# Kernel optimization log

Measured on AMD Instinct MI355X. Metric: run time of the kernel, lower is better.

Reference implementation:

```python
import jax, jax.numpy as jnp
import numpy as np

DIM = 128
NUM_HEADS = 4
HEAD_DIM = DIM // NUM_HEADS
WS = 8            # window height/width
SHIFT = 4
N_CAND = 4        # candidates per spatial position
H_RES, W_RES = 64, 128
M = WS * WS       # tokens per window spatially
L = M * N_CAND    # window sequence length
NW = (H_RES // WS) * (W_RES // WS)
B = 1
B_ = NW * B
NEG_INF = -1e9  # finite stand-in for -inf; softmax result identical within fp tolerance


def _rel_position_index():
    ch = np.arange(WS); cw = np.arange(WS)
    coords = np.stack(np.meshgrid(ch, cw, indexing='ij')).reshape(2, -1)  # [2, M]
    rel = (coords[:, :, None] - coords[:, None, :]).transpose(1, 2, 0)    # [M, M, 2]
    rel = rel + np.array([WS - 1, WS - 1])
    rel[..., 0] *= 2 * WS - 1
    return rel.sum(-1).astype(np.int32)  # [M, M] in [0, (2WS-1)^2)


def _window_attn_mask():
    # block message passing between same spatial position's candidates (except self)
    idx = np.repeat(np.arange(M), N_CAND).astype(np.float64)  # [L]
    m = idx[:, None] - idx[None, :]
    mask = np.where(m == 0, NEG_INF, 0.0)
    mask[np.arange(L), np.arange(L)] = 0.0
    return mask  # [L, L]


def _shift_window_attn_mask():
    img = np.zeros((H_RES, W_RES))
    cnt = 0
    for hs in (slice(0, -WS), slice(-WS, -SHIFT), slice(-SHIFT, None)):
        for ws in (slice(0, -WS), slice(-WS, -SHIFT), slice(-SHIFT, None)):
            img[hs, ws] = cnt
            cnt += 1
    mw = img.reshape(H_RES // WS, WS, W_RES // WS, WS).transpose(0, 2, 1, 3).reshape(-1, M)  # [nW, M]
    am = mw[:, None, :] - mw[:, :, None]           # [nW, M, M]
    am = np.where(am != 0, NEG_INF, 0.0)
    am = np.repeat(np.repeat(am, N_CAND, axis=1), N_CAND, axis=2)  # [nW, L, L]
    return am + _window_attn_mask()[None]


def setup_inputs() -> dict:
    key = jax.random.key(0)
    ks = jax.random.split(key, 6)
    x = jax.random.normal(ks[0], (B_, L, DIM), dtype=jnp.float32)
    qkv_w = jax.random.normal(ks[1], (3 * DIM, DIM), dtype=jnp.float32) * 0.02
    qkv_b = jnp.zeros((3 * DIM,), dtype=jnp.float32)
    rpe_table = jax.random.normal(ks[2], ((2 * WS - 1) ** 2, 3 * DIM), dtype=jnp.float32) * 0.02
    proj_w = jax.random.normal(ks[3], (DIM, DIM), dtype=jnp.float32) * 0.02
    proj_b = jnp.zeros((DIM,), dtype=jnp.float32)
    attn_mask = jnp.asarray(_shift_window_attn_mask(), dtype=jnp.float32)
    rel_idx = jnp.asarray(_rel_position_index())
    return {"x": x, "qkv_w": qkv_w, "qkv_b": qkv_b, "rpe_table": rpe_table,
            "proj_w": proj_w, "proj_b": proj_b, "attn_mask": attn_mask, "rel_idx": rel_idx}


def reference(x, qkv_w, qkv_b, rpe_table, proj_w, proj_b, attn_mask, rel_idx):
    b_, l, _ = x.shape
    h, hd = NUM_HEADS, HEAD_DIM
    scale = hd ** -0.5
    # QKV projection -> [B_, h, L, hd] each
    qkv = (x @ qkv_w.T + qkv_b).reshape(b_, l, 3, h, hd).transpose(2, 0, 3, 1, 4)
    q, k, v = qkv[0], qkv[1], qkv[2]
    # relative-position encodings gathered per (i, j) pair, expanded over candidates
    m = rel_idx.shape[0]
    n = l // m
    rpe = rpe_table[rel_idx.reshape(-1)].reshape(m, m, h, 3 * hd)
    rpe = jnp.repeat(jnp.repeat(rpe, n, axis=0), n, axis=1)  # [L, L, h, 3*hd]
    q_rpe, k_rpe, v_rpe = jnp.split(rpe, 3, axis=-1)
    q = q * scale
    q_rpe = q_rpe * scale
    qk = jnp.einsum('bhic,bhjc->bhij', q, k)
    qr = jnp.einsum('bhic,ijhc->bhij', q, k_rpe)
    kr = jnp.einsum('bhjc,ijhc->bhij', k, q_rpe)
    attn = qk + qr + kr  # [B_, h, L, L]
    nw = attn_mask.shape[0]
    attn = attn.reshape(b_ // nw, nw, h, l, l) + attn_mask[None, :, None]
    attn = attn.reshape(b_, h, l, l)
    attn = jax.nn.softmax(attn.astype(jnp.float32), axis=-1).astype(x.dtype)
    out = jnp.einsum('bhij,bhjc->bhic', attn, v) + jnp.einsum('bhij,ijhc->bhic', attn, v_rpe)
    out = out.transpose(0, 2, 1, 3).reshape(b_, l, DIM)
    return out @ proj_w.T + proj_b
```

## Files before the change

kernel.cpp:

```cpp
#include <hip/hip_runtime.h>
#include <math.h>

constexpr int HD    = 32;
constexpr int LW    = 256;
constexpr int NWIN  = 128;
constexpr int ROWS  = NWIN * LW;
constexpr int QKVC  = 384;
constexpr float SCALE = 0.17677669529663687f;

typedef __attribute__((ext_vector_type(8))) short short8;
typedef __attribute__((ext_vector_type(4))) float f32x4;
union I4S8 { int4 i; short8 s; };

__device__ inline float dot4(const float4 a, const float4 b) {
  return a.x * b.x + a.y * b.y + a.z * b.z + a.w * b.w;
}

__device__ inline unsigned short f2bf(float f) {
  unsigned u = __float_as_uint(f);
  unsigned r = (u + 0x7FFFu + ((u >> 16) & 1u)) >> 16;
  return (unsigned short)r;
}

__global__ __launch_bounds__(256) void cast_x4_kernel(
    const float* __restrict__ in, unsigned short* __restrict__ out, int n4)
{
  int i = blockIdx.x * 256 + threadIdx.x;
  if (i >= n4) return;
  float4 v = ((const float4*)in)[i];
  ushort4 o;
  o.x = f2bf(v.x); o.y = f2bf(v.y); o.z = f2bf(v.z); o.w = f2bf(v.w);
  ((ushort4*)out)[i] = o;
}

__global__ __launch_bounds__(256) void rpe_gather_kernel(
    const float* __restrict__ tab, const int* __restrict__ rel_idx,
    float* __restrict__ out)
{
  int gid = blockIdx.x * 256 + threadIdx.x;
  int s   = gid % 96;
  int hp  = gid / 96;
  int p   = hp & 4095;
  int h   = hp >> 12;
  float v = tab[(size_t)rel_idx[p] * 384 + h * 96 + s];
  if (s < 32) v *= SCALE;
  out[gid] = v;
}

template <int N>
__global__ __launch_bounds__(256) void gemm_mfma_bt(
    const unsigned short* __restrict__ A, const unsigned short* __restrict__ W,
    const float* __restrict__ bias, float* __restrict__ C)
{
  constexpr int K   = 128;
  constexpr int LDI = 28;
  __shared__ int As[128 * LDI];
  __shared__ int Bs[128 * LDI];
  const int tid  = threadIdx.x;
  const int wave = tid >> 6;
  const int lane = tid & 63;
  const int lm   = lane & 15;
  const int q    = lane >> 4;
  const int m0   = blockIdx.x * 128;
  const int n0   = blockIdx.y * 128;

  const int* Ag = (const int*)(A + (size_t)m0 * K);
  const int* Wg = (const int*)(W + (size_t)n0 * K);

  const int srow = tid >> 2;
  const int sk4  = (tid & 3) * 4;

  f32x4 acc[2][8] = {};

  for (int ks = 0; ks < 4; ++ks) {
    const int goff = ks * 16 + sk4;
    int4 a0 = *(const int4*)(Ag + (size_t)srow * 64 + goff);
    int4 a1 = *(const int4*)(Ag + (size_t)(srow + 64) * 64 + goff);
    int4 w0 = *(const int4*)(Wg + (size_t)srow * 64 + goff);
    int4 w1 = *(const int4*)(Wg + (size_t)(srow + 64) * 64 + goff);
    *(int4*)&As[srow * LDI + sk4]        = a0;
    *(int4*)&As[(srow + 64) * LDI + sk4] = a1;
    *(int4*)&Bs[srow * LDI + sk4]        = w0;
    *(int4*)&Bs[(srow + 64) * LDI + sk4] = w1;
    __syncthreads();

    short8 af[2], bf[8];
#pragma unroll
    for (int t = 0; t < 2; ++t) {
      const int m = (wave * 2 + t) * 16 + lm;
      I4S8 u; u.i = *(const int4*)&As[m * LDI + q * 4];
      af[t] = u.s;
    }
#pragma unroll
    for (int nt = 0; nt < 8; ++nt) {
      const int n = nt * 16 + lm;
      I4S8 u; u.i = *(const int4*)&Bs[n * LDI + q * 4];
      bf[nt] = u.s;
    }
#pragma unroll
    for (int t = 0; t < 2; ++t)
#pragma unroll
      for (int nt = 0; nt < 8; ++nt)
        acc[t][nt] = __builtin_amdgcn_mfma_f32_16x16x32_bf16(
            af[t], bf[nt], acc[t][nt], 0, 0, 0);
    __syncthreads();
  }

#pragma unroll
  for (int t = 0; t < 2; ++t) {
    const int mrow = m0 + (wave * 2 + t) * 16 + q * 4;
#pragma unroll
    for (int nt = 0; nt < 8; ++nt) {
      const int col = n0 + nt * 16 + lm;
      const float bb = bias[col];
#pragma unroll
      for (int r = 0; r < 4; ++r)
        C[(size_t)(mrow + r) * N + col] = acc[t][nt][r] + bb;
    }
  }
}

__global__ __launch_bounds__(512) void attn_kernel(
    const float* __restrict__ qkv, const float* __restrict__ rpeg,
    const float* __restrict__ mask, unsigned short* __restrict__ out)
{
  __shared__ float ms[256 * 33];
  const int b = blockIdx.x;
  const int h = blockIdx.y;
  const int tid = threadIdx.x;
  const int row = tid & 255;
  const int jh  = __builtin_amdgcn_readfirstlane(tid >> 8);
  const size_t rowbase = (size_t)b * LW;

  const float* kvbase = qkv + rowbase * QKVC + 128 + h * HD;

  float4 q[8];
  {
    const float4* qr = (const float4*)(qkv + (rowbase + row) * QKVC + h * HD);
#pragma unroll
    for (int d = 0; d < 8; ++d) {
      float4 t = qr[d];
      q[d] = make_float4(t.x * SCALE, t.y * SCALE, t.z * SCALE, t.w * SCALE);
    }
  }
  const float4* rp4base =
      (const float4*)(rpeg + ((size_t)h * 4096 + (size_t)(row >> 2) * 64) * 96);
  const float* mrow = mask + ((size_t)b * LW + row) * LW;

  float4 acc[8];
#pragma unroll
  for (int d = 0; d < 8; ++d) acc[d] = make_float4(0.f, 0.f, 0.f, 0.f);
  float l_run = 0.f;
  const int jbase = jh << 5;

  for (int l = 0; l < 32; ++l) {
    const int j4 = jbase + l;
    const float4* rp = rp4base + j4 * 24;
    float4 uq[8];
    float c0 = 0.f;
#pragma unroll
    for (int d = 0; d < 8; ++d) {
      float4 sq = rp[d];
      float4 kr = rp[8 + d];
      uq[d] = make_float4(q[d].x + sq.x, q[d].y + sq.y,
                          q[d].z + sq.z, q[d].w + sq.w);
      c0 += dot4(q[d], kr);
    }
    float4 mv = *(const float4*)(mrow + j4 * 4);
    const float* kj0 = kvbase + (size_t)(j4 * 4) * QKVC;
    float s[4] = {mv.x + c0, mv.y + c0, mv.z + c0, mv.w + c0};
#pragma unroll
    for (int jc = 0; jc < 4; ++jc) {
      const float4* kj = (const float4*)(kj0 + jc * QKVC);
      float sa = 0.f;
#pragma unroll
      for (int d = 0; d < 8; ++d) sa += dot4(uq[d], kj[d]);
      s[jc] += sa;
    }
    float p[4];
    p[0] = __expf(s[0]); p[1] = __expf(s[1]);
    p[2] = __expf(s[2]); p[3] = __expf(s[3]);
    float pool = (p[0] + p[1]) + (p[2] + p[3]);
    l_run += pool;
#pragma unroll
    for (int jc = 0; jc < 4; ++jc) {
      const float4* vj = (const float4*)(kj0 + jc * QKVC + 128);
      float pj = p[jc];
#pragma unroll
      for (int d = 0; d < 8; ++d) {
        acc[d].x += pj * vj[d].x; acc[d].y += pj * vj[d].y;
        acc[d].z += pj * vj[d].z; acc[d].w += pj * vj[d].w;
      }
    }
#pragma unroll
    for (int d = 0; d < 8; ++d) {
      float4 vr = rp[16 + d];
      acc[d].x += pool * vr.x; acc[d].y += pool * vr.y;
      acc[d].z += pool * vr.z; acc[d].w += pool * vr.w;
    }
  }

  __syncthreads();
  if (jh == 1) {
    float* dst = &ms[row * 33];
#pragma unroll
    for (int d = 0; d < 8; ++d) {
      dst[d * 4 + 0] = acc[d].x; dst[d * 4 + 1] = acc[d].y;
      dst[d * 4 + 2] = acc[d].z; dst[d * 4 + 3] = acc[d].w;
    }
    dst[32] = l_run;
  }
  __syncthreads();
  if (jh == 0) {
    const float* src = &ms[row * 33];
    float inv = 1.f / (l_run + src[32]);
    unsigned short* orow = out + (rowbase + row) * 128 + h * HD;
#pragma unroll
    for (int d = 0; d < 8; ++d) {
      ushort4 r;
      r.x = f2bf((acc[d].x + src[d * 4 + 0]) * inv);
      r.y = f2bf((acc[d].y + src[d * 4 + 1]) * inv);
      r.z = f2bf((acc[d].z + src[d * 4 + 2]) * inv);
      r.w = f2bf((acc[d].w + src[d * 4 + 3]) * inv);
      *(ushort4*)(orow + d * 4) = r;
    }
  }
}

extern "C" void kernel_launch(void* const* d_in, const int* in_sizes, int n_in,
                              void* d_out, int out_size, void* d_ws, size_t ws_size,
                              hipStream_t stream) {
  (void)in_sizes; (void)n_in; (void)out_size; (void)ws_size;
  const float* x         = (const float*)d_in[0];
  const float* qkv_w     = (const float*)d_in[1];
  const float* qkv_b     = (const float*)d_in[2];
  const float* rpe_table = (const float*)d_in[3];
  const float* proj_w    = (const float*)d_in[4];
  const float* proj_b    = (const float*)d_in[5];
  const float* attn_mask = (const float*)d_in[6];
  const int*   rel_idx   = (const int*)d_in[7];
  float* out = (float*)d_out;

  float* qkvbuf = (float*)d_ws;
  float* rpeg   = qkvbuf + (size_t)ROWS * QKVC;
  unsigned short* xbf    = (unsigned short*)(rpeg + (size_t)4 * 4096 * 96);
  unsigned short* qkvwbf = xbf + (size_t)ROWS * 128;
  unsigned short* projwbf= qkvwbf + (size_t)QKVC * 128;
  unsigned short* attnbf = projwbf + (size_t)128 * 128;

  hipLaunchKernelGGL(cast_x4_kernel, dim3(ROWS * 128 / 4 / 256), dim3(256), 0,
                     stream, x, xbf, ROWS * 128 / 4);
  hipLaunchKernelGGL(cast_x4_kernel, dim3(48), dim3(256), 0, stream,
                     qkv_w, qkvwbf, QKVC * 128 / 4);
  hipLaunchKernelGGL(cast_x4_kernel, dim3(16), dim3(256), 0, stream,
                     proj_w, projwbf, 128 * 128 / 4);
  hipLaunchKernelGGL(rpe_gather_kernel, dim3(6144), dim3(256), 0, stream,
                     rpe_table, rel_idx, rpeg);

  hipLaunchKernelGGL((gemm_mfma_bt<QKVC>), dim3(ROWS / 128, QKVC / 128),
                     dim3(256), 0, stream, xbf, qkvwbf, qkv_b, qkvbuf);
  hipLaunchKernelGGL(attn_kernel, dim3(NWIN, 4), dim3(512), 0, stream,
                     qkvbuf, rpeg, attn_mask, attnbf);
  hipLaunchKernelGGL((gemm_mfma_bt<128>), dim3(ROWS / 128, 1),
                     dim3(256), 0, stream, attnbf, projwbf, proj_b, out);
}
```

Before: 325.9 us.

## Decompose RPE attention into precomputed bias terms and MFMA score/PV kernel

Replaces the scalar fp32 attention kernel with a pipeline of separate kernels. The QKV GEMM now writes scaled Q, K and a transposed V in bf16, split per head. Two new kernels precompute the q·k_rpe and k·q_rpe bias tables. An MFMA kernel then computes QK^T and P·V, derives the shift-window and candidate mask from window indices instead of reading the mask tensor, and writes pooled probabilities. A finish kernel adds the v_rpe contribution and normalizes. The goal is to move the dominant FLOPs onto matrix cores and drop the 32MB mask read, at the cost of several large intermediate buffers and extra bf16 rounding of scores and biases.

```diff
diff --git a/kernel.cpp b/kernel.cpp
--- a/kernel.cpp
+++ b/kernel.cpp
@@ -1,7 +1,6 @@
 #include <hip/hip_runtime.h>
 #include <math.h>
 
-constexpr int HD    = 32;
 constexpr int LW    = 256;
 constexpr int NWIN  = 128;
 constexpr int ROWS  = NWIN * LW;
@@ -12,14 +11,12 @@
 typedef __attribute__((ext_vector_type(4))) float f32x4;
 union I4S8 { int4 i; short8 s; };
 
-__device__ inline float dot4(const float4 a, const float4 b) {
-  return a.x * b.x + a.y * b.y + a.z * b.z + a.w * b.w;
-}
-
 __device__ inline unsigned short f2bf(float f) {
   unsigned u = __float_as_uint(f);
-  unsigned r = (u + 0x7FFFu + ((u >> 16) & 1u)) >> 16;
-  return (unsigned short)r;
+  return (unsigned short)((u + 0x7FFFu + ((u >> 16) & 1u)) >> 16);
+}
+__device__ inline float bf2f(unsigned short s) {
+  return __uint_as_float(((unsigned)s) << 16);
 }
 
 __global__ __launch_bounds__(256) void cast_x4_kernel(
@@ -47,31 +44,25 @@
   out[gid] = v;
 }
 
-template <int N>
-__global__ __launch_bounds__(256) void gemm_mfma_bt(
+__global__ __launch_bounds__(256) void qkv_gemm(
     const unsigned short* __restrict__ A, const unsigned short* __restrict__ W,
-    const float* __restrict__ bias, float* __restrict__ C)
-{
-  constexpr int K   = 128;
-  constexpr int LDI = 28;
+    const float* __restrict__ bias,
+    unsigned short* __restrict__ qsbf, unsigned short* __restrict__ Kbf,
+    unsigned short* __restrict__ Vtg)
+{
+  constexpr int K = 128, LDI = 28;
   __shared__ int As[128 * LDI];
   __shared__ int Bs[128 * LDI];
-  const int tid  = threadIdx.x;
-  const int wave = tid >> 6;
-  const int lane = tid & 63;
-  const int lm   = lane & 15;
-  const int q    = lane >> 4;
-  const int m0   = blockIdx.x * 128;
-  const int n0   = blockIdx.y * 128;
-
+  const int tid = threadIdx.x, wave = tid >> 6, lane = tid & 63;
+  const int lm = lane & 15, q = lane >> 4;
+  const int m0 = blockIdx.x * 128;
+  const int region = blockIdx.y;
+  const int n0 = region * 128;
   const int* Ag = (const int*)(A + (size_t)m0 * K);
   const int* Wg = (const int*)(W + (size_t)n0 * K);
-
-  const int srow = tid >> 2;
-  const int sk4  = (tid & 3) * 4;
+  const int srow = tid >> 2, sk4 = (tid & 3) * 4;
 
   f32x4 acc[2][8] = {};
-
   for (int ks = 0; ks < 4; ++ks) {
     const int goff = ks * 16 + sk4;
     int4 a0 = *(const int4*)(Ag + (size_t)srow * 64 + goff);
@@ -83,7 +74,6 @@
     *(int4*)&Bs[srow * LDI + sk4]        = w0;
     *(int4*)&Bs[(srow + 64) * LDI + sk4] = w1;
     __syncthreads();
-
     short8 af[2], bf[8];
 #pragma unroll
     for (int t = 0; t < 2; ++t) {
@@ -105,7 +95,257 @@
             af[t], bf[nt], acc[t][nt], 0, 0, 0);
     __syncthreads();
   }
-
+#pragma unroll
+  for (int t = 0; t < 2; ++t) {
+#pragma unroll
+    for (int nt = 0; nt < 8; ++nt) {
+      const int c = nt * 16 + lm, hh = c >> 5, d = c & 31;
+      const float bb = bias[n0 + c];
+#pragma unroll
+      for (int r = 0; r < 4; ++r) {
+        const int ig = m0 + (wave * 2 + t) * 16 + q * 4 + r;
+        const int b = ig >> 8, i = ig & 255;
+        const size_t bh = (size_t)(b * 4 + hh);
+        const float v = acc[t][nt][r] + bb;
+        if (region == 0)      qsbf[(bh * 256 + i) * 32 + d] = f2bf(v * SCALE);
+        else if (region == 1) Kbf[(bh * 256 + i) * 32 + d]  = f2bf(v);
+        else                  Vtg[(bh * 32 + d) * 256 + i]  = f2bf(v);
+      }
+    }
+  }
+}
+
+__global__ __launch_bounds__(256) void c0_kernel(
+    const unsigned short* __restrict__ qsbf, const float* __restrict__ rpeg,
+    unsigned short* __restrict__ c0g)
+{
+  const int blk = blockIdx.x;
+  const int bq = blk & 7, hj = blk >> 3, h = hj >> 6, j4 = hj & 63;
+  const int b = bq * 16 + (threadIdx.x >> 4);
+  const int i0 = (threadIdx.x & 15) * 16;
+  const size_t bh = (size_t)(b * 4 + h);
+  unsigned short outb[16];
+  for (int ii = 0; ii < 16; ++ii) {
+    const int i = i0 + ii;
+    const float* kr = rpeg + ((size_t)h * 4096 + (size_t)(i >> 2) * 64 + j4) * 96 + 32;
+    const unsigned short* qr = qsbf + (bh * 256 + i) * 32;
+    float s = 0.f;
+#pragma unroll
+    for (int d4 = 0; d4 < 8; ++d4) {
+      ushort4 u = *(const ushort4*)(qr + d4 * 4);
+      float4 k = *(const float4*)(kr + d4 * 4);
+      s += bf2f(u.x) * k.x + bf2f(u.y) * k.y + bf2f(u.z) * k.z + bf2f(u.w) * k.w;
+    }
+    outb[ii] = f2bf(s);
+  }
+  unsigned short* dst = c0g + (((size_t)h * 128 + b) * 64 + j4) * 256 + i0;
+  *(int4*)(dst)     = *(int4*)&outb[0];
+  *(int4*)(dst + 8) = *(int4*)&outb[8];
+}
+
+__global__ __launch_bounds__(256) void t2_kernel(
+    const unsigned short* __restrict__ Kbf, const float* __restrict__ rpeg,
+    unsigned short* __restrict__ t2g)
+{
+  const int blk = blockIdx.x;
+  const int bq = blk & 7, hi = blk >> 3, h = hi >> 6, i4 = hi & 63;
+  const int b = bq * 16 + (threadIdx.x >> 4);
+  const int jg = threadIdx.x & 15;
+  const size_t bh = (size_t)(b * 4 + h);
+  unsigned short outb[16];
+  for (int jj = 0; jj < 16; ++jj) {
+    const int j = jg * 16 + jj;
+    const float* sq = rpeg + ((size_t)h * 4096 + (size_t)i4 * 64 + (j >> 2)) * 96;
+    const unsigned short* krow = Kbf + (bh * 256 + j) * 32;
+    float s = 0.f;
+#pragma unroll
+    for (int d4 = 0; d4 < 8; ++d4) {
+      ushort4 u = *(const ushort4*)(krow + d4 * 4);
+      float4 k = *(const float4*)(sq + d4 * 4);
+      s += bf2f(u.x) * k.x + bf2f(u.y) * k.y + bf2f(u.z) * k.z + bf2f(u.w) * k.w;
+    }
+    outb[jj] = f2bf(s);
+  }
+  unsigned short* dst = t2g + (((size_t)h * 128 + b) * 64 + i4) * 256 + jg * 16;
+  *(int4*)(dst)     = *(int4*)&outb[0];
+  *(int4*)(dst + 8) = *(int4*)&outb[8];
+}
+
+__global__ __launch_bounds__(1024) void attn_mfma(
+    const unsigned short* __restrict__ qsbf, const unsigned short* __restrict__ Kbf,
+    const unsigned short* __restrict__ Vtg, const unsigned short* __restrict__ c0g,
+    const unsigned short* __restrict__ t2g,
+    float* __restrict__ O_raw, float* __restrict__ lbuf,
+    unsigned short* __restrict__ poolg)
+{
+  __shared__ float Plds[16 * 576];
+  const int b = blockIdx.x, h = blockIdx.y;
+  const int tid = threadIdx.x, wave = tid >> 6, lane = tid & 63;
+  const int q = lane >> 4, lm = lane & 15;
+  const size_t bh = (size_t)(b * 4 + h);
+  const int ibase = wave * 16;
+
+  short8 qfrag;
+  { I4S8 u; u.i = *(const int4*)(qsbf + (bh * 256 + ibase + lm) * 32 + q * 8);
+    qfrag = u.s; }
+
+  const int bh7 = ((b >> 4) == 7) ? 1 : 0;
+  const int bw15 = ((b & 15) == 15) ? 1 : 0;
+  int ii[4], rid_i[4];
+#pragma unroll
+  for (int r = 0; r < 4; ++r) {
+    const int i = ibase + q * 4 + r; ii[r] = i;
+    const int m = i >> 2, mh = m >> 3, mw = m & 7;
+    rid_i[r] = (bh7 ? (mh >= 4 ? 2 : 1) : 0) * 3 + (bw15 ? (mw >= 4 ? 2 : 1) : 0);
+  }
+
+  f32x4 acc0 = {0.f, 0.f, 0.f, 0.f}, acc1 = {0.f, 0.f, 0.f, 0.f};
+  float lp[4] = {0.f, 0.f, 0.f, 0.f};
+  float* Pw = Plds + wave * 576;
+  const unsigned short* Kb  = Kbf + bh * 8192;
+  const unsigned short* Vb  = Vtg + bh * 8192;
+  const unsigned short* c0b = c0g + (size_t)(h * 128 + b) * 16384;
+  const unsigned short* t2b = t2g + (size_t)(h * 128 + b) * 16384;
+
+  for (int it = 0; it < 8; ++it) {
+    const int jb = it * 32;
+#pragma unroll
+    for (int jtt = 0; jtt < 2; ++jtt) {
+      const int jcol = jb + jtt * 16;
+      const int j = jcol + lm;
+      I4S8 ku; ku.i = *(const int4*)(Kb + j * 32 + q * 8);
+      f32x4 z = {0.f, 0.f, 0.f, 0.f};
+      f32x4 sacc = __builtin_amdgcn_mfma_f32_16x16x32_bf16(qfrag, ku.s, z, 0, 0, 0);
+      const int mj = j >> 2, mjh = mj >> 3, mjw = mj & 7;
+      const int rid_j =
+          (bh7 ? (mjh >= 4 ? 2 : 1) : 0) * 3 + (bw15 ? (mjw >= 4 ? 2 : 1) : 0);
+#pragma unroll
+      for (int r = 0; r < 4; ++r) {
+        const int i = ii[r];
+        float s = sacc[r] + bf2f(c0b[mj * 256 + i]) + bf2f(t2b[(i >> 2) * 256 + j]);
+        const bool blocked = (rid_i[r] != rid_j) || (((i >> 2) == mj) && (i != j));
+        float p = blocked ? 0.f : __expf(s);
+        lp[r] += p;
+        float pl = p + __shfl_xor(p, 1);
+        pl += __shfl_xor(pl, 2);
+        if ((lm & 3) == 0)
+          poolg[(bh * 256 + i) * 64 + (jcol >> 2) + (lm >> 2)] = f2bf(pl);
+        Pw[(q * 4 + r) * 36 + jtt * 16 + lm] = p;
+      }
+    }
+    float4 pfa = *(const float4*)(Pw + lm * 36 + q * 8);
+    float4 pfb = *(const float4*)(Pw + lm * 36 + q * 8 + 4);
+    short8 pa;
+    pa[0] = (short)f2bf(pfa.x); pa[1] = (short)f2bf(pfa.y);
+    pa[2] = (short)f2bf(pfa.z); pa[3] = (short)f2bf(pfa.w);
+    pa[4] = (short)f2bf(pfb.x); pa[5] = (short)f2bf(pfb.y);
+    pa[6] = (short)f2bf(pfb.z); pa[7] = (short)f2bf(pfb.w);
+    { I4S8 v0; v0.i = *(const int4*)(Vb + lm * 256 + jb + q * 8);
+      acc0 = __builtin_amdgcn_mfma_f32_16x16x32_bf16(pa, v0.s, acc0, 0, 0, 0);
+      I4S8 v1; v1.i = *(const int4*)(Vb + (16 + lm) * 256 + jb + q * 8);
+      acc1 = __builtin_amdgcn_mfma_f32_16x16x32_bf16(pa, v1.s, acc1, 0, 0, 0); }
+  }
+
+#pragma unroll
+  for (int r = 0; r < 4; ++r) {
+    float l = lp[r];
+    l += __shfl_xor(l, 1); l += __shfl_xor(l, 2);
+    l += __shfl_xor(l, 4); l += __shfl_xor(l, 8);
+    if (lm == 0) lbuf[bh * 256 + ii[r]] = l;
+    O_raw[(bh * 256 + ii[r]) * 32 + lm]      = acc0[r];
+    O_raw[(bh * 256 + ii[r]) * 32 + 16 + lm] = acc1[r];
+  }
+}
+
+__global__ __launch_bounds__(256) void finish_kernel(
+    const float* __restrict__ O_raw, const float* __restrict__ lbuf,
+    const unsigned short* __restrict__ poolg, const float* __restrict__ rpeg,
+    unsigned short* __restrict__ attnbf)
+{
+  const int b = blockIdx.x, h = blockIdx.y, i = threadIdx.x;
+  const size_t bh = (size_t)(b * 4 + h);
+  const float inv = 1.f / lbuf[bh * 256 + i];
+  float pool[64];
+  { const ushort4* pp = (const ushort4*)(poolg + (bh * 256 + i) * 64);
+#pragma unroll
+    for (int t = 0; t < 16; ++t) {
+      ushort4 u = pp[t];
+      pool[t * 4 + 0] = bf2f(u.x); pool[t * 4 + 1] = bf2f(u.y);
+      pool[t * 4 + 2] = bf2f(u.z); pool[t * 4 + 3] = bf2f(u.w);
+    } }
+  float4 acc[8] = {};
+  const float* vbase = rpeg + ((size_t)h * 4096 + (size_t)(i >> 2) * 64) * 96 + 64;
+  for (int j4 = 0; j4 < 64; ++j4) {
+    const float pl = pool[j4];
+    const float4* vr = (const float4*)(vbase + (size_t)j4 * 96);
+#pragma unroll
+    for (int d4 = 0; d4 < 8; ++d4) {
+      float4 v = vr[d4];
+      acc[d4].x += pl * v.x; acc[d4].y += pl * v.y;
+      acc[d4].z += pl * v.z; acc[d4].w += pl * v.w;
+    }
+  }
+  const float4* orow = (const float4*)(O_raw + (bh * 256 + i) * 32);
+  unsigned short* dst = attnbf + ((size_t)b * 256 + i) * 128 + h * 32;
+#pragma unroll
+  for (int d4 = 0; d4 < 8; ++d4) {
+    float4 o = orow[d4];
+    ushort4 u;
+    u.x = f2bf((o.x + acc[d4].x) * inv);
+    u.y = f2bf((o.y + acc[d4].y) * inv);
+    u.z = f2bf((o.z + acc[d4].z) * inv);
+    u.w = f2bf((o.w + acc[d4].w) * inv);
+    *(ushort4*)(dst + d4 * 4) = u;
+  }
+}
+
+template <int N>
+__global__ __launch_bounds__(256) void gemm_mfma_bt(
+    const unsigned short* __restrict__ A, const unsigned short* __restrict__ W,
+    const float* __restrict__ bias, float* __restrict__ C)
+{
+  constexpr int K = 128, LDI = 28;
+  __shared__ int As[128 * LDI];
+  __shared__ int Bs[128 * LDI];
+  const int tid = threadIdx.x, wave = tid >> 6, lane = tid & 63;
+  const int lm = lane & 15, q = lane >> 4;
+  const int m0 = blockIdx.x * 128, n0 = blockIdx.y * 128;
+  const int* Ag = (const int*)(A + (size_t)m0 * K);
+  const int* Wg = (const int*)(W + (size_t)n0 * K);
+  const int srow = tid >> 2, sk4 = (tid & 3) * 4;
+  f32x4 acc[2][8] = {};
+  for (int ks = 0; ks < 4; ++ks) {
+    const int goff = ks * 16 + sk4;
+    int4 a0 = *(const int4*)(Ag + (size_t)srow * 64 + goff);
+    int4 a1 = *(const int4*)(Ag + (size_t)(srow + 64) * 64 + goff);
+    int4 w0 = *(const int4*)(Wg + (size_t)srow * 64 + goff);
+    int4 w1 = *(const int4*)(Wg + (size_t)(srow + 64) * 64 + goff);
+    *(int4*)&As[srow * LDI + sk4]        = a0;
+    *(int4*)&As[(srow + 64) * LDI + sk4] = a1;
+    *(int4*)&Bs[srow * LDI + sk4]        = w0;
+    *(int4*)&Bs[(srow + 64) * LDI + sk4] = w1;
+    __syncthreads();
+    short8 af[2], bf[8];
+#pragma unroll
+    for (int t = 0; t < 2; ++t) {
+      const int m = (wave * 2 + t) * 16 + lm;
+      I4S8 u; u.i = *(const int4*)&As[m * LDI + q * 4];
+      af[t] = u.s;
+    }
+#pragma unroll
+    for (int nt = 0; nt < 8; ++nt) {
+      const int n = nt * 16 + lm;
+      I4S8 u; u.i = *(const int4*)&Bs[n * LDI + q * 4];
+      bf[nt] = u.s;
+    }
+#pragma unroll
+    for (int t = 0; t < 2; ++t)
+#pragma unroll
+      for (int nt = 0; nt < 8; ++nt)
+        acc[t][nt] = __builtin_amdgcn_mfma_f32_16x16x32_bf16(
+            af[t], bf[nt], acc[t][nt], 0, 0, 0);
+    __syncthreads();
+  }
 #pragma unroll
   for (int t = 0; t < 2; ++t) {
     const int mrow = m0 + (wave * 2 + t) * 16 + q * 4;
@@ -116,113 +356,6 @@
 #pragma unroll
       for (int r = 0; r < 4; ++r)
         C[(size_t)(mrow + r) * N + col] = acc[t][nt][r] + bb;
-    }
-  }
-}
-
-__global__ __launch_bounds__(512) void attn_kernel(
-    const float* __restrict__ qkv, const float* __restrict__ rpeg,
-    const float* __restrict__ mask, unsigned short* __restrict__ out)
-{
-  __shared__ float ms[256 * 33];
-  const int b = blockIdx.x;
-  const int h = blockIdx.y;
-  const int tid = threadIdx.x;
-  const int row = tid & 255;
-  const int jh  = __builtin_amdgcn_readfirstlane(tid >> 8);
-  const size_t rowbase = (size_t)b * LW;
-
-  const float* kvbase = qkv + rowbase * QKVC + 128 + h * HD;
-
-  float4 q[8];
-  {
-    const float4* qr = (const float4*)(qkv + (rowbase + row) * QKVC + h * HD);
-#pragma unroll
-    for (int d = 0; d < 8; ++d) {
-      float4 t = qr[d];
-      q[d] = make_float4(t.x * SCALE, t.y * SCALE, t.z * SCALE, t.w * SCALE);
-    }
-  }
-  const float4* rp4base =
-      (const float4*)(rpeg + ((size_t)h * 4096 + (size_t)(row >> 2) * 64) * 96);
-  const float* mrow = mask + ((size_t)b * LW + row) * LW;
-
-  float4 acc[8];
-#pragma unroll
-  for (int d = 0; d < 8; ++d) acc[d] = make_float4(0.f, 0.f, 0.f, 0.f);
-  float l_run = 0.f;
-  const int jbase = jh << 5;
-
-  for (int l = 0; l < 32; ++l) {
-    const int j4 = jbase + l;
-    const float4* rp = rp4base + j4 * 24;
-    float4 uq[8];
-    float c0 = 0.f;
-#pragma unroll
-    for (int d = 0; d < 8; ++d) {
-      float4 sq = rp[d];
-      float4 kr = rp[8 + d];
-      uq[d] = make_float4(q[d].x + sq.x, q[d].y + sq.y,
-                          q[d].z + sq.z, q[d].w + sq.w);
-      c0 += dot4(q[d], kr);
-    }
-    float4 mv = *(const float4*)(mrow + j4 * 4);
-    const float* kj0 = kvbase + (size_t)(j4 * 4) * QKVC;
-    float s[4] = {mv.x + c0, mv.y + c0, mv.z + c0, mv.w + c0};
-#pragma unroll
-    for (int jc = 0; jc < 4; ++jc) {
-      const float4* kj = (const float4*)(kj0 + jc * QKVC);
-      float sa = 0.f;
-#pragma unroll
-      for (int d = 0; d < 8; ++d) sa += dot4(uq[d], kj[d]);
-      s[jc] += sa;
-    }
-    float p[4];
-    p[0] = __expf(s[0]); p[1] = __expf(s[1]);
-    p[2] = __expf(s[2]); p[3] = __expf(s[3]);
-    float pool = (p[0] + p[1]) + (p[2] + p[3]);
-    l_run += pool;
-#pragma unroll
-    for (int jc = 0; jc < 4; ++jc) {
-      const float4* vj = (const float4*)(kj0 + jc * QKVC + 128);
-      float pj = p[jc];
-#pragma unroll
-      for (int d = 0; d < 8; ++d) {
-        acc[d].x += pj * vj[d].x; acc[d].y += pj * vj[d].y;
-        acc[d].z += pj * vj[d].z; acc[d].w += pj * vj[d].w;
-      }
-    }
-#pragma unroll
-    for (int d = 0; d < 8; ++d) {
-      float4 vr = rp[16 + d];
-      acc[d].x += pool * vr.x; acc[d].y += pool * vr.y;
-      acc[d].z += pool * vr.z; acc[d].w += pool * vr.w;
-    }
-  }
-
-  __syncthreads();
-  if (jh == 1) {
-    float* dst = &ms[row * 33];
-#pragma unroll
-    for (int d = 0; d < 8; ++d) {
-      dst[d * 4 + 0] = acc[d].x; dst[d * 4 + 1] = acc[d].y;
-      dst[d * 4 + 2] = acc[d].z; dst[d * 4 + 3] = acc[d].w;
-    }
-    dst[32] = l_run;
-  }
-  __syncthreads();
-  if (jh == 0) {
-    const float* src = &ms[row * 33];
-    float inv = 1.f / (l_run + src[32]);
-    unsigned short* orow = out + (rowbase + row) * 128 + h * HD;
-#pragma unroll
-    for (int d = 0; d < 8; ++d) {
-      ushort4 r;
-      r.x = f2bf((acc[d].x + src[d * 4 + 0]) * inv);
-      r.y = f2bf((acc[d].y + src[d * 4 + 1]) * inv);
-      r.z = f2bf((acc[d].z + src[d * 4 + 2]) * inv);
-      r.w = f2bf((acc[d].w + src[d * 4 + 3]) * inv);
-      *(ushort4*)(orow + d * 4) = r;
     }
   }
 }
@@ -237,30 +370,42 @@
   const float* rpe_table = (const float*)d_in[3];
   const float* proj_w    = (const float*)d_in[4];
   const float* proj_b    = (const float*)d_in[5];
-  const float* attn_mask = (const float*)d_in[6];
   const int*   rel_idx   = (const int*)d_in[7];
   float* out = (float*)d_out;
 
-  float* qkvbuf = (float*)d_ws;
-  float* rpeg   = qkvbuf + (size_t)ROWS * QKVC;
-  unsigned short* xbf    = (unsigned short*)(rpeg + (size_t)4 * 4096 * 96);
-  unsigned short* qkvwbf = xbf + (size_t)ROWS * 128;
-  unsigned short* projwbf= qkvwbf + (size_t)QKVC * 128;
-  unsigned short* attnbf = projwbf + (size_t)128 * 128;
-
-  hipLaunchKernelGGL(cast_x4_kernel, dim3(ROWS * 128 / 4 / 256), dim3(256), 0,
-                     stream, x, xbf, ROWS * 128 / 4);
+  char* w = (char*)d_ws;
+  unsigned short* xbf     = (unsigned short*)w;            w += 8388608;
+  unsigned short* qkvwbf  = (unsigned short*)w;            w += 98304;
+  unsigned short* projwbf = (unsigned short*)w;            w += 32768;
+  float*          rpeg    = (float*)w;                     w += 6291456;
+  unsigned short* qsbf    = (unsigned short*)w;            w += 8388608;
+  unsigned short* Kbf     = (unsigned short*)w;            w += 8388608;
+  unsigned short* Vtg     = (unsigned short*)w;            w += 8388608;
+  unsigned short* c0g     = (unsigned short*)w;            w += 16777216;
+  unsigned short* t2g     = (unsigned short*)w;            w += 16777216;
+  unsigned short* poolg   = (unsigned short*)w;            w += 16777216;
+  float*          O_raw   = (float*)w;                     w += 16777216;
+  float*          lbuf    = (float*)w;                     w += 524288;
+  unsigned short* attnbf  = xbf;
+
+  hipLaunchKernelGGL(cast_x4_kernel, dim3(4096), dim3(256), 0, stream,
+                     x, xbf, ROWS * 128 / 4);
   hipLaunchKernelGGL(cast_x4_kernel, dim3(48), dim3(256), 0, stream,
                      qkv_w, qkvwbf, QKVC * 128 / 4);
   hipLaunchKernelGGL(cast_x4_kernel, dim3(16), dim3(256), 0, stream,
                      proj_w, projwbf, 128 * 128 / 4);
   hipLaunchKernelGGL(rpe_gather_kernel, dim3(6144), dim3(256), 0, stream,
                      rpe_table, rel_idx, rpeg);
-
-  hipLaunchKernelGGL((gemm_mfma_bt<QKVC>), dim3(ROWS / 128, QKVC / 128),
-                     dim3(256), 0, stream, xbf, qkvwbf, qkv_b, qkvbuf);
-  hipLaunchKernelGGL(attn_kernel, dim3(NWIN, 4), dim3(512), 0, stream,
-                     qkvbuf, rpeg, attn_mask, attnbf);
-  hipLaunchKernelGGL((gemm_mfma_bt<128>), dim3(ROWS / 128, 1),
-                     dim3(256), 0, stream, attnbf, projwbf, proj_b, out);
-}
+  hipLaunchKernelGGL(qkv_gemm, dim3(ROWS / 128, 3), dim3(256), 0, stream,
+                     xbf, qkvwbf, qkv_b, qsbf, Kbf, Vtg);
+  hipLaunchKernelGGL(c0_kernel, dim3(2048), dim3(256), 0, stream,
+                     qsbf, rpeg, c0g);
+  hipLaunchKernelGGL(t2_kernel, dim3(2048), dim3(256), 0, stream,
+                     Kbf, rpeg, t2g);
+  hipLaunchKernelGGL(attn_mfma, dim3(NWIN, 4), dim3(1024), 0, stream,
+                     qsbf, Kbf, Vtg, c0g, t2g, O_raw, lbuf, poolg);
+  hipLaunchKernelGGL(finish_kernel, dim3(NWIN, 4), dim3(256), 0, stream,
+                     O_raw, lbuf, poolg, rpeg, attnbf);
+  hipLaunchKernelGGL((gemm_mfma_bt<128>), dim3(ROWS / 128, 1), dim3(256), 0,
+                     stream, attnbf, projwbf, proj_b, out);
+}
```

Measured after the change: 556.5 us. 70.8% more time.
